# Optimization experiments

Hardware: AMD Instinct MI355X
Metric: run time of the kernel (lower is better)

Reference implementation:

```python
import jax, jax.numpy as jnp
import numpy as np

N = 20000      # nodes
E = 640000     # edges
FIN = 256
FQK = 256


def setup_inputs() -> dict:
    key = jax.random.key(0)
    kx, ks, kd, kw = jax.random.split(key, 4)
    x = jax.random.normal(kx, (N, FIN), dtype=jnp.float32)
    # src must be sorted (original scatter_softmax assumes grouped index);
    # force last element to N-1 so nbatches == N as in batch[-1]+1.
    src = jnp.sort(jax.random.randint(ks, (E,), 0, N))
    src = src.at[-1].set(N - 1)
    dest = jax.random.randint(kd, (E,), 0, N)
    ei = jnp.stack([src, dest]).astype(jnp.int64)
    # nn.Linear(Fin, 2*Fqk, bias=False) weight: [2*Fqk, Fin]
    bound = 1.0 / np.sqrt(FIN)
    W = jax.random.uniform(kw, (2 * FQK, FIN), dtype=jnp.float32,
                           minval=-bound, maxval=bound)
    return {"x": x, "ei": ei, "W": W}


def reference(x, ei, W):
    src, dest = ei[0], ei[1]
    n_nodes = x.shape[0]
    scaling = FQK ** -0.5
    qk = x @ W.T                      # [N, 2*Fqk]
    q, k = jnp.split(qk, 2, axis=-1)  # each [N, Fqk]
    q = q * scaling
    # per-edge dot product: (q[src] . k[dest])  -> [E]
    aw = jnp.einsum('ef,ef->e', q[src], k[dest])
    # scatter softmax over edges grouped by src node (raw exp, as original)
    ex = jnp.exp(aw)
    expsum = jax.ops.segment_sum(ex, src, num_segments=n_nodes)  # [N]
    return ex / expsum[src]
```

## Files before the change

kernel.cpp:

```cpp
#include <hip/hip_runtime.h>
#include <cmath>

#define FIN 256
#define FQK 256
#define SCALING 0.0625f
#define MAX_SEG 256
#define ASTRIDE 264

typedef _Float16 f16_t;
typedef f16_t f16x8 __attribute__((ext_vector_type(8)));
typedef f16_t f16x2 __attribute__((ext_vector_type(2)));
typedef float f32x4 __attribute__((ext_vector_type(4)));

__device__ __forceinline__ f16x8 cvt8h(float4 a, float4 b) {
    f16x8 r;
    r[0] = (f16_t)a.x; r[1] = (f16_t)a.y; r[2] = (f16_t)a.z; r[3] = (f16_t)a.w;
    r[4] = (f16_t)b.x; r[5] = (f16_t)b.y; r[6] = (f16_t)b.z; r[7] = (f16_t)b.w;
    return r;
}

__device__ __forceinline__ float fdot2f(f16x2 a, f16x2 b, float c) {
#if __has_builtin(__builtin_amdgcn_fdot2)
    return __builtin_amdgcn_fdot2(a, b, c, false);
#else
    return c + (float)a[0] * (float)b[0] + (float)a[1] * (float)b[1];
#endif
}

union H16 { uint4 u; f16x2 h[4]; };
__device__ __forceinline__ float dot16(uint4 ya, uint4 xa, float acc) {
    H16 A; A.u = ya;
    H16 X; X.u = xa;
#pragma unroll
    for (int i = 0; i < 4; ++i) acc = fdot2f(A.h[i], X.h[i], acc);
    return acc;
}

__global__ __launch_bounds__(256) void m_seg_kernel(const float* __restrict__ W,
                                                    f16_t* __restrict__ MbF,
                                                    const int* __restrict__ src,
                                                    int* __restrict__ seg, int N, int E) {
    const int b = blockIdx.x;
    if (b < FIN) {
        const int f = b;
        const int k = threadIdx.x;
        const float* __restrict__ Wq = W;
        const float* __restrict__ Wk = W + FQK * FIN;
        float acc = 0.f;
#pragma unroll 8
        for (int c = 0; c < FQK; ++c)
            acc += Wq[c * FIN + f] * Wk[c * FIN + k];
        const int ft  = f >> 4, m16 = f & 15;
        const int kcI = k >> 5, q = (k >> 3) & 3, e = k & 7;
        MbF[(size_t)(((kcI * 16 + ft) * 64 + q * 16 + m16) * 8 + e)] =
            (f16_t)(acc * SCALING);
    } else {
        const int n = (b - FIN) * 256 + threadIdx.x;
        if (n > N) return;
        int lo = 0, hi = E;
        while (lo < hi) {
            const int mid = (lo + hi) >> 1;
            if (src[mid] < n) lo = mid + 1; else hi = mid;
        }
        seg[n] = lo;
    }
}

__global__ __launch_bounds__(256) void gemm_y_kernel(const float* __restrict__ x,
                                                     const f16_t* __restrict__ MbF,
                                                     f16_t* __restrict__ y,
                                                     f16_t* __restrict__ xh, int N) {
    __shared__ f16_t sA[16 * ASTRIDE];

    const int t    = threadIdx.x;
    const int wv   = t >> 6;
    const int lane = t & 63;
    const int q    = lane >> 4;
    const int m16  = lane & 15;
    const int n0   = blockIdx.x * 16;
    const int f0   = wv * 64;

    {
        const int rsub = t >> 5;
        const int col  = (t & 31) * 8;
#pragma unroll
        for (int p = 0; p < 2; ++p) {
            const int r  = p * 8 + rsub;
            const int n  = n0 + r;
            const int nc = n < N ? n : N - 1;
            const float* __restrict__ xp = x + (size_t)nc * FIN + col;
            const float4 a = *(const float4*)(xp);
            const float4 b = *(const float4*)(xp + 4);
            const f16x8 v = cvt8h(a, b);
            *(f16x8*)&sA[r * ASTRIDE + col] = v;
            if (n < N) *(f16x8*)(xh + (size_t)n * FIN + col) = v;
        }
    }
    __syncthreads();

    f32x4 acc[4] = {};

#pragma unroll
    for (int kc = 0; kc < FIN; kc += 32) {
        const f16x8 af = *(const f16x8*)&sA[m16 * ASTRIDE + kc + q * 8];
        const f16_t* __restrict__ bp =
            MbF + (size_t)(((kc >> 5) * 16 + (f0 >> 4)) * 64 + lane) * 8;
#pragma unroll
        for (int ft = 0; ft < 4; ++ft) {
            union { uint4 u; f16x8 v; } bu;
            bu.u = *(const uint4*)(bp + ft * 512);
            acc[ft] = __builtin_amdgcn_mfma_f32_16x16x32_f16(af, bu.v, acc[ft], 0, 0, 0);
        }
    }

    __syncthreads();
#pragma unroll
    for (int ft = 0; ft < 4; ++ft)
#pragma unroll
        for (int r = 0; r < 4; ++r)
            sA[(q * 4 + r) * ASTRIDE + f0 + ft * 16 + m16] = (f16_t)acc[ft][r];
    __syncthreads();

    {
        const int row = t >> 4;
        const int c   = (t & 15) * 16;
        const int n   = n0 + row;
        if (n < N) {
            const uint4 v0 = *(const uint4*)&sA[row * ASTRIDE + c];
            const uint4 v1 = *(const uint4*)&sA[row * ASTRIDE + c + 8];
            *(uint4*)(y + (size_t)n * FIN + c)     = v0;
            *(uint4*)(y + (size_t)n * FIN + c + 8) = v1;
        }
    }
}

__global__ __launch_bounds__(256) void node_edge_kernel(const f16_t* __restrict__ xh,
                                                        const f16_t* __restrict__ y,
                                                        const int* __restrict__ dest,
                                                        const int* __restrict__ seg,
                                                        float* __restrict__ out,
                                                        int N, int E, int nwaves) {
    __shared__ float exlds[4][MAX_SEG];

    const int w    = threadIdx.x >> 6;
    const int lane = threadIdx.x & 63;
    const int g    = lane >> 3;
    const int j    = lane & 7;

#define DCLAMP(d) ((unsigned)(d) < (unsigned)N ? (d) : 0)

#define GISSUE(B0, B1, B2, B3, dval, valid)                                    \
    if (valid) {                                                               \
        const int d_ = DCLAMP(dval);                                           \
        const uint4* __restrict__ yr = (const uint4*)(y + (size_t)d_ * FIN);   \
        B0 = yr[j]; B1 = yr[8 + j]; B2 = yr[16 + j]; B3 = yr[24 + j];          \
    }

#define CONSUME(B0, B1, B2, B3, idx, valid)                                    \
    if (valid) {                                                               \
        float a_ = 0.f;                                                        \
        a_ = dot16(B0, X0, a_);                                                \
        a_ = dot16(B1, X1, a_);                                                \
        a_ = dot16(B2, X2, a_);                                                \
        a_ = dot16(B3, X3, a_);                                                \
        a_ += __shfl_xor(a_, 1, 64);                                           \
        a_ += __shfl_xor(a_, 2, 64);                                           \
        a_ += __shfl_xor(a_, 4, 64);                                           \
        const float ex = __expf(a_);                                           \
        sum += ex;                                                             \
        if (j == 0 && (idx) < MAX_SEG) exlds[w][idx] = ex;                     \
    }

    for (int n = blockIdx.x * 4 + w; n < N; n += nwaves) {
        int s0 = seg[n], s1 = seg[n + 1];
        s0 = min(max(s0, 0), E);
        s1 = min(max(s1, 0), E);
        const int cnt = s1 - s0;
        if (cnt <= 0) continue;

        const uint4* __restrict__ xp = (const uint4*)(xh + (size_t)n * FIN);
        const uint4 X0 = xp[j], X1 = xp[8 + j], X2 = xp[16 + j], X3 = xp[24 + j];

        float sum = 0.f;
        const int nit = (cnt + 7) >> 3;

        uint4 A0, A1, A2, A3, B0, B1, B2, B3;

        bool vA = g < cnt;
        int  dA = vA ? dest[s0 + g] : 0;
        GISSUE(A0, A1, A2, A3, dA, vA);
        bool vBn = (8 + g) < cnt;
        int  dB  = vBn ? dest[s0 + 8 + g] : 0;

        for (int it = 0; it < nit; it += 2) {
            const int  iB = (it + 1) * 8 + g;
            const bool vB = iB < cnt;
            GISSUE(B0, B1, B2, B3, dB, vB);
            const int  iA2 = (it + 2) * 8 + g;
            const bool vA2 = iA2 < cnt;
            dA = vA2 ? dest[s0 + iA2] : 0;
            CONSUME(A0, A1, A2, A3, it * 8 + g, vA);
            GISSUE(A0, A1, A2, A3, dA, vA2);
            const int  iB3 = (it + 3) * 8 + g;
            const bool vB3 = iB3 < cnt;
            dB = vB3 ? dest[s0 + iB3] : 0;
            CONSUME(B0, B1, B2, B3, iB, vB);
            vA = vA2;
        }

        sum += __shfl_xor(sum, 8, 64);
        sum += __shfl_xor(sum, 16, 64);
        sum += __shfl_xor(sum, 32, 64);
        const float inv = 1.0f / sum;

        const int lim = cnt < MAX_SEG ? cnt : MAX_SEG;
        for (int i = lane; i < lim; i += 64)
            out[s0 + i] = exlds[w][i] * inv;
    }

#undef GISSUE
#undef CONSUME
#undef DCLAMP
}

extern "C" void kernel_launch(void* const* d_in, const int* in_sizes, int n_in,
                              void* d_out, int out_size, void* d_ws, size_t ws_size,
                              hipStream_t stream) {
    const float* x  = (const float*)d_in[0];
    const int*   ei = (const int*)d_in[1];
    const float* W  = (const float*)d_in[2];
    float* out = (float*)d_out;

    const int N = in_sizes[0] / FIN;
    const int E = in_sizes[1] / 2;

    f16_t* MbF = (f16_t*)d_ws;
    f16_t* y   = MbF + (size_t)FIN * FIN;
    f16_t* xh  = y + (size_t)N * FIN;
    int*   seg = (int*)(xh + (size_t)N * FIN);

    const int segBlocks = (N + 256) / 256;
    m_seg_kernel<<<FIN + segBlocks, 256, 0, stream>>>(W, MbF, ei, seg, N, E);

    gemm_y_kernel<<<(N + 15) / 16, 256, 0, stream>>>(x, MbF, y, xh, N);

    const int neBlocks = 2048;
    node_edge_kernel<<<neBlocks, 256, 0, stream>>>(xh, y, ei + E, seg, out,
                                                   N, E, neBlocks * 4);
}
```

Baseline: 130.9 us.

## Double GEMM row tile to 32 and move segment search into GEMM launch

The GEMM block now covers 32 node rows instead of 16, so each wave issues two MFMA row tiles per B fragment and reuses each B load twice. The segment-offset binary search moves out of the M-matrix kernel into extra blocks of the GEMM launch. The aim is to halve B-matrix global traffic per output and shorten the small first kernel. The cost is fewer GEMM blocks, more accumulator registers and twice the shared memory per block.

After: 132.3 us. Within noise of the previous version (+1.1%).

```diff
diff --git a/kernel.cpp b/kernel.cpp
--- a/kernel.cpp
+++ b/kernel.cpp
@@ -36,26 +36,33 @@
     return acc;
 }
 
-__global__ __launch_bounds__(256) void m_seg_kernel(const float* __restrict__ W,
-                                                    f16_t* __restrict__ MbF,
-                                                    const int* __restrict__ src,
-                                                    int* __restrict__ seg, int N, int E) {
-    const int b = blockIdx.x;
-    if (b < FIN) {
-        const int f = b;
-        const int k = threadIdx.x;
-        const float* __restrict__ Wq = W;
-        const float* __restrict__ Wk = W + FQK * FIN;
-        float acc = 0.f;
+__global__ __launch_bounds__(256) void m_kernel(const float* __restrict__ W,
+                                                f16_t* __restrict__ MbF) {
+    const int f = blockIdx.x;
+    const int k = threadIdx.x;
+    const float* __restrict__ Wq = W;
+    const float* __restrict__ Wk = W + FQK * FIN;
+    float acc = 0.f;
 #pragma unroll 8
-        for (int c = 0; c < FQK; ++c)
-            acc += Wq[c * FIN + f] * Wk[c * FIN + k];
-        const int ft  = f >> 4, m16 = f & 15;
-        const int kcI = k >> 5, q = (k >> 3) & 3, e = k & 7;
-        MbF[(size_t)(((kcI * 16 + ft) * 64 + q * 16 + m16) * 8 + e)] =
-            (f16_t)(acc * SCALING);
-    } else {
-        const int n = (b - FIN) * 256 + threadIdx.x;
+    for (int c = 0; c < FQK; ++c)
+        acc += Wq[c * FIN + f] * Wk[c * FIN + k];
+    const int ft  = f >> 4, m16 = f & 15;
+    const int kcI = k >> 5, q = (k >> 3) & 3, e = k & 7;
+    MbF[(size_t)(((kcI * 16 + ft) * 64 + q * 16 + m16) * 8 + e)] =
+        (f16_t)(acc * SCALING);
+}
+
+__global__ __launch_bounds__(256) void gemm_seg_kernel(const float* __restrict__ x,
+                                                       const f16_t* __restrict__ MbF,
+                                                       f16_t* __restrict__ y,
+                                                       f16_t* __restrict__ xh,
+                                                       const int* __restrict__ src,
+                                                       int* __restrict__ seg,
+                                                       int N, int E, int GB) {
+    const int t = threadIdx.x;
+
+    if (blockIdx.x >= GB) {
+        const int n = (blockIdx.x - GB) * 256 + t;
         if (n > N) return;
         int lo = 0, hi = E;
         while (lo < hi) {
@@ -63,28 +70,23 @@
             if (src[mid] < n) lo = mid + 1; else hi = mid;
         }
         seg[n] = lo;
-    }
-}
-
-__global__ __launch_bounds__(256) void gemm_y_kernel(const float* __restrict__ x,
-                                                     const f16_t* __restrict__ MbF,
-                                                     f16_t* __restrict__ y,
-                                                     f16_t* __restrict__ xh, int N) {
-    __shared__ f16_t sA[16 * ASTRIDE];
-
-    const int t    = threadIdx.x;
+        return;
+    }
+
+    __shared__ f16_t sA[32 * ASTRIDE];
+
     const int wv   = t >> 6;
     const int lane = t & 63;
     const int q    = lane >> 4;
     const int m16  = lane & 15;
-    const int n0   = blockIdx.x * 16;
+    const int n0   = blockIdx.x * 32;
     const int f0   = wv * 64;
 
     {
         const int rsub = t >> 5;
         const int col  = (t & 31) * 8;
 #pragma unroll
-        for (int p = 0; p < 2; ++p) {
+        for (int p = 0; p < 4; ++p) {
             const int r  = p * 8 + rsub;
             const int n  = n0 + r;
             const int nc = n < N ? n : N - 1;
@@ -98,31 +100,42 @@
     }
     __syncthreads();
 
-    f32x4 acc[4] = {};
+    f32x4 acc[2][4] = {};
 
 #pragma unroll
     for (int kc = 0; kc < FIN; kc += 32) {
-        const f16x8 af = *(const f16x8*)&sA[m16 * ASTRIDE + kc + q * 8];
+        f16x8 afrag[2];
+#pragma unroll
+        for (int mt = 0; mt < 2; ++mt)
+            afrag[mt] = *(const f16x8*)&sA[(mt * 16 + m16) * ASTRIDE + kc + q * 8];
+
         const f16_t* __restrict__ bp =
             MbF + (size_t)(((kc >> 5) * 16 + (f0 >> 4)) * 64 + lane) * 8;
 #pragma unroll
         for (int ft = 0; ft < 4; ++ft) {
             union { uint4 u; f16x8 v; } bu;
             bu.u = *(const uint4*)(bp + ft * 512);
-            acc[ft] = __builtin_amdgcn_mfma_f32_16x16x32_f16(af, bu.v, acc[ft], 0, 0, 0);
+#pragma unroll
+            for (int mt = 0; mt < 2; ++mt)
+                acc[mt][ft] = __builtin_amdgcn_mfma_f32_16x16x32_f16(afrag[mt], bu.v,
+                                                                    acc[mt][ft], 0, 0, 0);
         }
     }
 
     __syncthreads();
 #pragma unroll
-    for (int ft = 0; ft < 4; ++ft)
-#pragma unroll
-        for (int r = 0; r < 4; ++r)
-            sA[(q * 4 + r) * ASTRIDE + f0 + ft * 16 + m16] = (f16_t)acc[ft][r];
+    for (int mt = 0; mt < 2; ++mt)
+#pragma unroll
+        for (int ft = 0; ft < 4; ++ft)
+#pragma unroll
+            for (int r = 0; r < 4; ++r)
+                sA[(mt * 16 + q * 4 + r) * ASTRIDE + f0 + ft * 16 + m16] =
+                    (f16_t)acc[mt][ft][r];
     __syncthreads();
 
-    {
-        const int row = t >> 4;
+#pragma unroll
+    for (int s = 0; s < 2; ++s) {
+        const int row = s * 16 + (t >> 4);
         const int c   = (t & 15) * 16;
         const int n   = n0 + row;
         if (n < N) {
@@ -239,10 +252,11 @@
     f16_t* xh  = y + (size_t)N * FIN;
     int*   seg = (int*)(xh + (size_t)N * FIN);
 
-    const int segBlocks = (N + 256) / 256;
-    m_seg_kernel<<<FIN + segBlocks, 256, 0, stream>>>(W, MbF, ei, seg, N, E);
-
-    gemm_y_kernel<<<(N + 15) / 16, 256, 0, stream>>>(x, MbF, y, xh, N);
+    m_kernel<<<FIN, 256, 0, stream>>>(W, MbF);
+
+    const int GB   = (N + 31) / 32;
+    const int segB = (N + 256) / 256;
+    gemm_seg_kernel<<<GB + segB, 256, 0, stream>>>(x, MbF, y, xh, ei, seg, N, E, GB);
 
     const int neBlocks = 2048;
     node_edge_kernel<<<neBlocks, 256, 0, stream>>>(xh, y, ei + E, seg, out,
```
